# Kernel tuning notes

Hardware: AMD Instinct MI355X
Metric: run time of the kernel (lower is better)

## Reference

```python
import jax, jax.numpy as jnp
import numpy as np

B, C, K, P, STRIDE, ITERS = 32, 32, 3, 4, 1, 3
PSIZE = P * P
EPS = 1e-6


def unfold_patches(x, K, stride):
    # Replicates F.unfold(x_chw, kernel_size=K, padding=K//2, stride=stride)
    # followed by transpose(1,2).view(b, oh, ow, K*K, c) — including the
    # channel-major flat ordering that the view reinterprets.
    b, h, w, c = x.shape
    pad = K // 2
    xp = jnp.pad(jnp.transpose(x, (0, 3, 1, 2)), ((0, 0), (0, 0), (pad, pad), (pad, pad)))
    oh = (h + 2 * pad - K) // stride + 1
    ow = (w + 2 * pad - K) // stride + 1
    rows = []
    for ki in range(K):
        cols = []
        for kj in range(K):
            cols.append(xp[:, :, ki:ki + (oh - 1) * stride + 1:stride, kj:kj + (ow - 1) * stride + 1:stride])
        rows.append(jnp.stack(cols, axis=2))  # (b, c, K, oh, ow)
    pat = jnp.stack(rows, axis=2)  # (b, c, K, K, oh, ow)
    pat = pat.reshape(b, c * K * K, oh * ow)  # unfold output (b, c*K*K, L)
    pat = jnp.transpose(pat, (0, 2, 1)).reshape(b, oh, ow, K * K, c)
    return pat, oh, ow


def squash(s, eps=EPS):
    s2 = jnp.sum(s * s, axis=-1, keepdims=True)
    return (s2 / (1.0 + s2)) * s / jnp.sqrt(s2 + eps)


def dynamic_routing(v, a_in, iters=ITERS, eps=EPS):
    # v: (n, in_votes, C, psize), a_in: (n, in_votes, 1)
    n, in_votes, Cc, _ = v.shape
    b_ij = jnp.zeros((n, in_votes, Cc), dtype=v.dtype)
    a_in = jnp.clip(a_in, 0.0001, 1.0)
    v_j = None
    for t in range(iters):
        c_ij = jax.nn.softmax(b_ij, axis=2) * a_in
        c_ij = c_ij / (jnp.sum(c_ij, axis=2, keepdims=True) + eps)
        s_j = jnp.einsum('nic,nicq->ncq', c_ij, v)
        v_j = squash(s_j)
        if t < iters - 1:
            agreement = jnp.einsum('nicq,ncq->nic', v, v_j)
            b_ij = b_ij + agreement
    a_out = jnp.clip(jnp.sqrt(jnp.sum(v_j * v_j, axis=-1) + eps), 0.0001, 1.0 - 0.0001)
    return v_j, a_out


def setup_inputs() -> dict:
    key = jax.random.key(0)
    k1, k2 = jax.random.split(key)
    x = jax.random.normal(k1, (2, 14, 14, B * (PSIZE + 1)), dtype=jnp.float32)
    weights = jax.random.normal(k2, (K * K * B, C, PSIZE, PSIZE), dtype=jnp.float32) * 0.02
    return {"x": x, "weights": weights}


def reference(x, weights):
    b, h, w, c = x.shape
    patches, oh, ow = unfold_patches(x, K, STRIDE)
    p_in = patches[..., :B * PSIZE].reshape(b * oh * ow, K * K * B, PSIZE)
    a_in = patches[..., B * PSIZE:].reshape(b * oh * ow, K * K * B, 1)
    votes = jnp.einsum('bip,icpq->bicq', p_in, weights)  # (n, KKB, C, psize)
    p_vec, a_vec = dynamic_routing(votes, a_in)
    p_out = p_vec.reshape(b, oh, ow, C * PSIZE)
    a_out = a_vec.reshape(b, oh, ow, C)
    out = jnp.concatenate([p_out, a_out], axis=3)
    p_out = jnp.nan_to_num(p_out, nan=0.0, posinf=10000.0, neginf=-10000.0)
    a_out = jnp.nan_to_num(a_out, nan=0.5, posinf=1.0 - 0.0001, neginf=0.0001)
    out = jnp.nan_to_num(out, nan=0.0, posinf=10000.0, neginf=-10000.0)
    return p_out, a_out, out
```

## Files before the change

### kernel.cpp

```cpp
#include <hip/hip_runtime.h>
#include <hip/hip_fp16.h>
#include <math.h>

#define NB 392
#define NI 288
#define NC 32
#define NQ 16
#define CQ 512
#define CH 544
#define EPSV 1e-6f

#define VSCALE 32.0f
#define VINV (1.0f / 32.0f)

#define OFF_AOUT 200704
#define OFF_CAT  213248

#define RT_THREADS 512
#define RT_WAVES 8

typedef _Float16 v4h __attribute__((ext_vector_type(4)));
typedef float v4f __attribute__((ext_vector_type(4)));
typedef float v2f __attribute__((ext_vector_type(2)));

__device__ __forceinline__ float gather_x(const float* __restrict__ x, int n, int j) {
    int c_idx = j / 9;
    int rem = j - c_idx * 9;
    int ki = rem / 3;
    int kj = rem - ki * 3;
    int b_ = n / 196;
    int rest = n - b_ * 196;
    int yy = rest / 14;
    int xx = rest - yy * 14;
    int iy = yy + ki - 1;
    int ix = xx + kj - 1;
    float v = 0.f;
    if ((unsigned)iy < 14u && (unsigned)ix < 14u)
        v = x[((b_ * 14 + iy) * 14 + ix) * CH + c_idx];
    return v;
}

__global__ __launch_bounds__(256) void votes_k(const float* __restrict__ x,
                                               const float* __restrict__ wts,
                                               uchar* __restrict__ votes) {
    __shared__ _Float16 wlds[8192];
    __shared__ uint tile[64 * 36];
    int mtt = blockIdx.x;
    int i = blockIdx.y;
    int t = threadIdx.x;
    int wv = t >> 6;
    int l = t & 63;
    int col = l & 15;
    int quad = l >> 4;

    const float* wsrc = wts + (size_t)i * 8192;
#pragma unroll
    for (int k = 0; k < 8; ++k) {
        int f0 = k * 1024 + t * 4;
        float4 w4 = *(const float4*)(wsrc + f0);
        int ct = f0 >> 8;
        int p = (f0 >> 4) & 15;
        int qd = p >> 2;
        int kk = p & 3;
        int q0 = f0 & 15;
        int s = (ct * 4 + qd) & 15;
        int base = ct * 256 + qd * 64 + kk;
        wlds[base + (((q0 + 0) ^ s) << 2)] = (_Float16)(w4.x * VSCALE);
        wlds[base + (((q0 + 1) ^ s) << 2)] = (_Float16)(w4.y * VSCALE);
        wlds[base + (((q0 + 2) ^ s) << 2)] = (_Float16)(w4.z * VSCALE);
        wlds[base + (((q0 + 3) ^ s) << 2)] = (_Float16)(w4.w * VSCALE);
    }

    int n_row = mtt * 64 + wv * 16 + col;
    v4h av = {};
    if (n_row < NB) {
        int jb = (i >> 5) * CH + (i & 31) * 16 + quad * 4;
#pragma unroll
        for (int kk = 0; kk < 4; ++kk)
            av[kk] = (_Float16)gather_x(x, n_row, jb + kk);
    }
    __syncthreads();

    const uchar* tileb = (const uchar*)tile;

    for (int ch = 0; ch < 4; ++ch) {
#pragma unroll
        for (int c8 = 0; c8 < 8; ++c8) {
            int ct = ch * 8 + c8;
            v4h bv = *(const v4h*)&wlds[ct * 256 + quad * 64 +
                                        ((col ^ ((ct * 4 + quad) & 15)) << 2)];
            v4f acc = {0.f, 0.f, 0.f, 0.f};
            acc = __builtin_amdgcn_mfma_f32_16x16x16f16(bv, av, acc, 0, 0, 0);
            uint u = __builtin_amdgcn_cvt_pk_fp8_f32(acc[0], acc[1], 0, false);
            u = __builtin_amdgcn_cvt_pk_fp8_f32(acc[2], acc[3], u, true);
            tile[(wv * 16 + col) * 36 + c8 * 4 + quad] = u;
        }
        __syncthreads();
#pragma unroll
        for (int k = 0; k < 2; ++k) {
            int idx = k * 256 + t;
            int row = idx >> 3;
            int off = idx & 7;
            int n_out = mtt * 64 + row;
            if (n_out < NB) {
                uint4 d = *(const uint4*)&tileb[row * 144 + off * 16];
                *(uint4*)(votes + (((size_t)n_out * NI + i) << 9) + ch * 128 + off * 16) = d;
            }
        }
        __syncthreads();
    }
}

__global__ __launch_bounds__(RT_THREADS) void routing_k(const uchar* __restrict__ votes,
                                                        const float* __restrict__ x,
                                                        float* __restrict__ out) {
    __shared__ float afs[NI];
    __shared__ float sred[RT_WAVES * CQ];
    __shared__ float vj[CQ];
    __shared__ float aout_s[NC];

    int n = blockIdx.x;
    int t = threadIdx.x;
    int wv = t >> 6;
    int l = t & 63;
    int c = l & 31;
    int g = l >> 5;

    if (t < NI) {
        int j = (t >> 5) * CH + 512 + (t & 31);
        float v = gather_x(x, n, j);
        float a = fminf(fmaxf(v, 1e-4f), 1.0f);
        afs[t] = a / (a + EPSV);
    }
    __syncthreads();

    const uchar* vb = votes + (size_t)n * NI * 512;
    float vjr[16];
    float sreg[16];

#define VROW(S) (((const uint4*)(vb + ((size_t)(((((S) << 3) + wv) << 1) + g) << 9)))[c])

    for (int iter = 0; iter < 3; ++iter) {
#pragma unroll
        for (int q = 0; q < 16; ++q) sreg[q] = 0.f;

        uint4 f0 = VROW(0), f1 = VROW(1), f2 = VROW(2), f3 = VROW(3);

#pragma clang loop unroll_count(2)
        for (int s = 0; s < 18; ++s) {
            int i = ((s << 3) + wv) * 2 + g;
            uint4 cur = f0;
            f0 = f1; f1 = f2; f2 = f3;
            if (s + 4 < 18) f3 = VROW(s + 4);

            float vt[16];
            {
                v2f p;
                p = __builtin_amdgcn_cvt_pk_f32_fp8(cur.x, false); vt[0] = p[0];  vt[1] = p[1];
                p = __builtin_amdgcn_cvt_pk_f32_fp8(cur.x, true);  vt[2] = p[0];  vt[3] = p[1];
                p = __builtin_amdgcn_cvt_pk_f32_fp8(cur.y, false); vt[4] = p[0];  vt[5] = p[1];
                p = __builtin_amdgcn_cvt_pk_f32_fp8(cur.y, true);  vt[6] = p[0];  vt[7] = p[1];
                p = __builtin_amdgcn_cvt_pk_f32_fp8(cur.z, false); vt[8] = p[0];  vt[9] = p[1];
                p = __builtin_amdgcn_cvt_pk_f32_fp8(cur.z, true);  vt[10] = p[0]; vt[11] = p[1];
                p = __builtin_amdgcn_cvt_pk_f32_fp8(cur.w, false); vt[12] = p[0]; vt[13] = p[1];
                p = __builtin_amdgcn_cvt_pk_f32_fp8(cur.w, true);  vt[14] = p[0]; vt[15] = p[1];
            }
            float cij;
            if (iter == 0) {
                cij = afs[i] * (1.0f / 32.0f);
            } else {
                float ah = 0.f;
#pragma unroll
                for (int q = 0; q < 16; ++q) ah += vt[q] * vjr[q];
                float e = __expf(ah);
                float ssum = e;
                ssum += __shfl_xor(ssum, 1);
                ssum += __shfl_xor(ssum, 2);
                ssum += __shfl_xor(ssum, 4);
                ssum += __shfl_xor(ssum, 8);
                ssum += __shfl_xor(ssum, 16);
                cij = e * __builtin_amdgcn_rcpf(ssum) * afs[i];
            }
#pragma unroll
            for (int q = 0; q < 16; ++q) sreg[q] += cij * vt[q];
        }

#pragma unroll
        for (int q = 0; q < 16; ++q) sreg[q] += __shfl_xor(sreg[q], 32);
        if (g == 0) {
            float* sw = &sred[wv * CQ + c];
#pragma unroll
            for (int q = 0; q < 16; ++q) sw[q * 32] = sreg[q];
        }
        __syncthreads();
        {
            float ssum = 0.f;
#pragma unroll
            for (int k = 0; k < RT_WAVES; ++k) ssum += sred[k * CQ + t];
            sred[t] = ssum * VINV;
        }
        __syncthreads();

        if (t < NC) {
            float s2 = 0.f;
#pragma unroll
            for (int q = 0; q < 16; ++q) {
                float s = sred[q * 32 + t];
                s2 += s * s;
            }
            float f = (s2 / (1.f + s2)) / sqrtf(s2 + EPSV);
            float vn2 = 0.f;
#pragma unroll
            for (int q = 0; q < 16; ++q) {
                float v = f * sred[q * 32 + t];
                vj[q * 32 + t] = v;
                vn2 += v * v;
            }
            if (iter == 2) {
                float ao = sqrtf(vn2 + EPSV);
                ao = fminf(fmaxf(ao, 1e-4f), 1.f - 1e-4f);
                aout_s[t] = ao;
            }
        }
        __syncthreads();
        if (iter < 2) {
#pragma unroll
            for (int q = 0; q < 16; ++q) {
                float v = vj[q * 32 + c] * VINV;
                vjr[q] = (iter == 0) ? v : vjr[q] + v;
            }
        }
    }

    {
        float v = vj[(t & 15) * 32 + (t >> 4)];
        out[(size_t)n * CQ + t] = v;
        out[OFF_CAT + (size_t)n * 544 + t] = v;
    }
    if (t < NC) {
        float ao = aout_s[t];
        out[OFF_AOUT + n * 32 + t] = ao;
        out[OFF_CAT + (size_t)n * 544 + 512 + t] = ao;
    }
}

extern "C" void kernel_launch(void* const* d_in, const int* in_sizes, int n_in,
                              void* d_out, int out_size, void* d_ws, size_t ws_size,
                              hipStream_t stream) {
    const float* x = (const float*)d_in[0];
    const float* wts = (const float*)d_in[1];
    float* out = (float*)d_out;
    uchar* votes = (uchar*)d_ws;

    hipLaunchKernelGGL(votes_k, dim3(7, NI), dim3(256), 0, stream,
                       x, wts, votes);
    hipLaunchKernelGGL(routing_k, dim3(NB), dim3(RT_THREADS), 0, stream,
                       votes, x, out);
}
```

Before: 114.6 us.

## Fuse votes and routing into one persistent kernel with a global barrier

Merges the votes and routing kernels into one 392-block kernel. Each block first computes a contiguous slice of the 2016 votes tiles, full 32 capsules per tile, reloading weights only when the input index changes. An atomic-counter grid barrier then separates this from the routing phase, which reuses the shared memory through a union. This removes the second kernel launch and the inter-kernel gap, but adds a memset, a spin barrier that relies on all blocks being co-resident, and less parallelism in the votes phase.

```diff
diff --git a/kernel.cpp b/kernel.cpp
--- a/kernel.cpp
+++ b/kernel.cpp
@@ -9,6 +9,8 @@
 #define CQ 512
 #define CH 544
 #define EPSV 1e-6f
+#define NTILE 2016
+#define NBLK 392
 
 #define VSCALE 32.0f
 #define VINV (1.0f / 32.0f)
@@ -16,8 +18,10 @@
 #define OFF_AOUT 200704
 #define OFF_CAT  213248
 
-#define RT_THREADS 512
+#define FK_THREADS 512
 #define RT_WAVES 8
+#define TILE_PITCH 132
+#define FLAG_OFF (64u << 20)
 
 typedef _Float16 v4h __attribute__((ext_vector_type(4)));
 typedef float v4f __attribute__((ext_vector_type(4)));
@@ -40,89 +44,115 @@
     return v;
 }
 
-__global__ __launch_bounds__(256) void votes_k(const float* __restrict__ x,
-                                               const float* __restrict__ wts,
-                                               uchar* __restrict__ votes) {
-    __shared__ _Float16 wlds[8192];
-    __shared__ uint tile[64 * 36];
-    int mtt = blockIdx.x;
-    int i = blockIdx.y;
+union SMem {
+    struct {
+        _Float16 wlds[8192];
+        uint tile[64 * TILE_PITCH];
+    } a;
+    struct {
+        float afs[NI];
+        float sred[RT_WAVES * CQ];
+        float vj[CQ];
+        float aout_s[NC];
+    } b;
+};
+
+__global__ __launch_bounds__(FK_THREADS, 4) void fused_k(const float* __restrict__ x,
+                                                         const float* __restrict__ wts,
+                                                         uchar* __restrict__ votes,
+                                                         uint* __restrict__ flag,
+                                                         float* __restrict__ out) {
+    __shared__ SMem sm;
+
+    int b = blockIdx.x;
     int t = threadIdx.x;
     int wv = t >> 6;
     int l = t & 63;
     int col = l & 15;
     int quad = l >> 4;
 
-    const float* wsrc = wts + (size_t)i * 8192;
-#pragma unroll
-    for (int k = 0; k < 8; ++k) {
-        int f0 = k * 1024 + t * 4;
-        float4 w4 = *(const float4*)(wsrc + f0);
-        int ct = f0 >> 8;
-        int p = (f0 >> 4) & 15;
-        int qd = p >> 2;
-        int kk = p & 3;
-        int q0 = f0 & 15;
-        int s = (ct * 4 + qd) & 15;
-        int base = ct * 256 + qd * 64 + kk;
-        wlds[base + (((q0 + 0) ^ s) << 2)] = (_Float16)(w4.x * VSCALE);
-        wlds[base + (((q0 + 1) ^ s) << 2)] = (_Float16)(w4.y * VSCALE);
-        wlds[base + (((q0 + 2) ^ s) << 2)] = (_Float16)(w4.z * VSCALE);
-        wlds[base + (((q0 + 3) ^ s) << 2)] = (_Float16)(w4.w * VSCALE);
-    }
-
-    int n_row = mtt * 64 + wv * 16 + col;
-    v4h av = {};
-    if (n_row < NB) {
-        int jb = (i >> 5) * CH + (i & 31) * 16 + quad * 4;
-#pragma unroll
-        for (int kk = 0; kk < 4; ++kk)
-            av[kk] = (_Float16)gather_x(x, n_row, jb + kk);
-    }
+    {
+        int start = (b * NTILE) / NBLK;
+        int end = ((b + 1) * NTILE) / NBLK;
+        int cur_i = -1;
+        int rloc = wv & 3;
+        int cthalf = wv >> 2;
+
+        for (int id = start; id < end; ++id) {
+            int i = id / 7;
+            int mtt = id - i * 7;
+
+            if (i != cur_i) {
+                const float* wsrc = wts + (size_t)i * 8192;
+#pragma unroll
+                for (int k = 0; k < 4; ++k) {
+                    int f0 = k * 2048 + t * 4;
+                    float4 w4 = *(const float4*)(wsrc + f0);
+                    int ct = f0 >> 8;
+                    int p = (f0 >> 4) & 15;
+                    int qd = p >> 2;
+                    int kk = p & 3;
+                    int q0 = f0 & 15;
+                    int s = (ct * 4 + qd) & 15;
+                    int base = ct * 256 + qd * 64 + kk;
+                    sm.a.wlds[base + (((q0 + 0) ^ s) << 2)] = (_Float16)(w4.x * VSCALE);
+                    sm.a.wlds[base + (((q0 + 1) ^ s) << 2)] = (_Float16)(w4.y * VSCALE);
+                    sm.a.wlds[base + (((q0 + 2) ^ s) << 2)] = (_Float16)(w4.z * VSCALE);
+                    sm.a.wlds[base + (((q0 + 3) ^ s) << 2)] = (_Float16)(w4.w * VSCALE);
+                }
+                cur_i = i;
+                __syncthreads();
+            }
+
+            int n_row = mtt * 64 + rloc * 16 + col;
+            v4h av = {};
+            if (n_row < NB) {
+                int jb = (i >> 5) * CH + (i & 31) * 16 + quad * 4;
+#pragma unroll
+                for (int kk = 0; kk < 4; ++kk)
+                    av[kk] = (_Float16)gather_x(x, n_row, jb + kk);
+            }
+
+#pragma unroll
+            for (int cc = 0; cc < 16; ++cc) {
+                int ct = cthalf * 16 + cc;
+                v4h bv = *(const v4h*)&sm.a.wlds[ct * 256 + quad * 64 +
+                                                ((col ^ ((ct * 4 + quad) & 15)) << 2)];
+                v4f acc = {0.f, 0.f, 0.f, 0.f};
+                acc = __builtin_amdgcn_mfma_f32_16x16x16f16(bv, av, acc, 0, 0, 0);
+                uint u = __builtin_amdgcn_cvt_pk_fp8_f32(acc[0], acc[1], 0, false);
+                u = __builtin_amdgcn_cvt_pk_fp8_f32(acc[2], acc[3], u, true);
+                sm.a.tile[(rloc * 16 + col) * TILE_PITCH + ct * 4 + quad] = u;
+            }
+            __syncthreads();
+
+            const uchar* tileb = (const uchar*)sm.a.tile;
+#pragma unroll
+            for (int k = 0; k < 4; ++k) {
+                int idx = k * 512 + t;
+                int row = idx >> 5;
+                int off = idx & 31;
+                int n_out = mtt * 64 + row;
+                if (n_out < NB) {
+                    uint4 d = *(const uint4*)&tileb[row * (TILE_PITCH * 4) + off * 16];
+                    *(uint4*)(votes + (((size_t)n_out * NI + i) << 9) + off * 16) = d;
+                }
+            }
+            __syncthreads();
+        }
+    }
+
+    __threadfence();
     __syncthreads();
-
-    const uchar* tileb = (const uchar*)tile;
-
-    for (int ch = 0; ch < 4; ++ch) {
-#pragma unroll
-        for (int c8 = 0; c8 < 8; ++c8) {
-            int ct = ch * 8 + c8;
-            v4h bv = *(const v4h*)&wlds[ct * 256 + quad * 64 +
-                                        ((col ^ ((ct * 4 + quad) & 15)) << 2)];
-            v4f acc = {0.f, 0.f, 0.f, 0.f};
-            acc = __builtin_amdgcn_mfma_f32_16x16x16f16(bv, av, acc, 0, 0, 0);
-            uint u = __builtin_amdgcn_cvt_pk_fp8_f32(acc[0], acc[1], 0, false);
-            u = __builtin_amdgcn_cvt_pk_fp8_f32(acc[2], acc[3], u, true);
-            tile[(wv * 16 + col) * 36 + c8 * 4 + quad] = u;
-        }
-        __syncthreads();
-#pragma unroll
-        for (int k = 0; k < 2; ++k) {
-            int idx = k * 256 + t;
-            int row = idx >> 3;
-            int off = idx & 7;
-            int n_out = mtt * 64 + row;
-            if (n_out < NB) {
-                uint4 d = *(const uint4*)&tileb[row * 144 + off * 16];
-                *(uint4*)(votes + (((size_t)n_out * NI + i) << 9) + ch * 128 + off * 16) = d;
-            }
-        }
-        __syncthreads();
-    }
-}
-
-__global__ __launch_bounds__(RT_THREADS) void routing_k(const uchar* __restrict__ votes,
-                                                        const float* __restrict__ x,
-                                                        float* __restrict__ out) {
-    __shared__ float afs[NI];
-    __shared__ float sred[RT_WAVES * CQ];
-    __shared__ float vj[CQ];
-    __shared__ float aout_s[NC];
-
-    int n = blockIdx.x;
-    int t = threadIdx.x;
-    int wv = t >> 6;
-    int l = t & 63;
+    if (t == 0) {
+        __hip_atomic_fetch_add(flag, 1u, __ATOMIC_RELEASE, __HIP_MEMORY_SCOPE_AGENT);
+        while (__hip_atomic_load(flag, __ATOMIC_ACQUIRE, __HIP_MEMORY_SCOPE_AGENT) < NBLK)
+            __builtin_amdgcn_s_sleep(16);
+    }
+    __syncthreads();
+    __threadfence();
+
+    int n = b;
     int c = l & 31;
     int g = l >> 5;
 
@@ -130,7 +160,7 @@
         int j = (t >> 5) * CH + 512 + (t & 31);
         float v = gather_x(x, n, j);
         float a = fminf(fmaxf(v, 1e-4f), 1.0f);
-        afs[t] = a / (a + EPSV);
+        sm.b.afs[t] = a / (a + EPSV);
     }
     __syncthreads();
 
@@ -167,7 +197,7 @@
             }
             float cij;
             if (iter == 0) {
-                cij = afs[i] * (1.0f / 32.0f);
+                cij = sm.b.afs[i] * (1.0f / 32.0f);
             } else {
                 float ah = 0.f;
 #pragma unroll
@@ -179,7 +209,7 @@
                 ssum += __shfl_xor(ssum, 4);
                 ssum += __shfl_xor(ssum, 8);
                 ssum += __shfl_xor(ssum, 16);
-                cij = e * __builtin_amdgcn_rcpf(ssum) * afs[i];
+                cij = e * __builtin_amdgcn_rcpf(ssum) * sm.b.afs[i];
             }
 #pragma unroll
             for (int q = 0; q < 16; ++q) sreg[q] += cij * vt[q];
@@ -188,7 +218,7 @@
 #pragma unroll
         for (int q = 0; q < 16; ++q) sreg[q] += __shfl_xor(sreg[q], 32);
         if (g == 0) {
-            float* sw = &sred[wv * CQ + c];
+            float* sw = &sm.b.sred[wv * CQ + c];
 #pragma unroll
             for (int q = 0; q < 16; ++q) sw[q * 32] = sreg[q];
         }
@@ -196,8 +226,8 @@
         {
             float ssum = 0.f;
 #pragma unroll
-            for (int k = 0; k < RT_WAVES; ++k) ssum += sred[k * CQ + t];
-            sred[t] = ssum * VINV;
+            for (int k = 0; k < RT_WAVES; ++k) ssum += sm.b.sred[k * CQ + t];
+            sm.b.sred[t] = ssum * VINV;
         }
         __syncthreads();
 
@@ -205,40 +235,40 @@
             float s2 = 0.f;
 #pragma unroll
             for (int q = 0; q < 16; ++q) {
-                float s = sred[q * 32 + t];
+                float s = sm.b.sred[q * 32 + t];
                 s2 += s * s;
             }
             float f = (s2 / (1.f + s2)) / sqrtf(s2 + EPSV);
             float vn2 = 0.f;
 #pragma unroll
             for (int q = 0; q < 16; ++q) {
-                float v = f * sred[q * 32 + t];
-                vj[q * 32 + t] = v;
+                float v = f * sm.b.sred[q * 32 + t];
+                sm.b.vj[q * 32 + t] = v;
                 vn2 += v * v;
             }
             if (iter == 2) {
                 float ao = sqrtf(vn2 + EPSV);
                 ao = fminf(fmaxf(ao, 1e-4f), 1.f - 1e-4f);
-                aout_s[t] = ao;
+                sm.b.aout_s[t] = ao;
             }
         }
         __syncthreads();
         if (iter < 2) {
 #pragma unroll
             for (int q = 0; q < 16; ++q) {
-                float v = vj[q * 32 + c] * VINV;
+                float v = sm.b.vj[q * 32 + c] * VINV;
                 vjr[q] = (iter == 0) ? v : vjr[q] + v;
             }
         }
     }
 
     {
-        float v = vj[(t & 15) * 32 + (t >> 4)];
+        float v = sm.b.vj[(t & 15) * 32 + (t >> 4)];
         out[(size_t)n * CQ + t] = v;
         out[OFF_CAT + (size_t)n * 544 + t] = v;
     }
     if (t < NC) {
-        float ao = aout_s[t];
+        float ao = sm.b.aout_s[t];
         out[OFF_AOUT + n * 32 + t] = ao;
         out[OFF_CAT + (size_t)n * 544 + 512 + t] = ao;
     }
@@ -251,9 +281,10 @@
     const float* wts = (const float*)d_in[1];
     float* out = (float*)d_out;
     uchar* votes = (uchar*)d_ws;
-
-    hipLaunchKernelGGL(votes_k, dim3(7, NI), dim3(256), 0, stream,
-                       x, wts, votes);
-    hipLaunchKernelGGL(routing_k, dim3(NB), dim3(RT_THREADS), 0, stream,
-                       votes, x, out);
+    uint* flag = (uint*)((uchar*)d_ws + FLAG_OFF);
+
+    hipMemsetAsync(flag, 0, sizeof(uint), stream);
+
+    hipLaunchKernelGGL(fused_k, dim3(NBLK), dim3(FK_THREADS), 0, stream,
+                       x, wts, votes, flag, out);
 }
```

New measurement: 319.3 us. 2.79x slower.
